# Kernel tuning notes

Measured on AMD Instinct MI355X. Metric: run time of the kernel, lower is better.

The kernel has to match this reference:

```python
import jax, jax.numpy as jnp
import numpy as np
import math

HID = 300   # model dim (d_k in the source's scale factor)
HDIM = 64   # attention projection dim
NH = 8      # heads = last axis of view(B,S,HDIM//8,8)
DH = HDIM // NH
L = 6


def pos_encoding(S, d):
    pos = jnp.arange(S, dtype=jnp.float32)[:, None]
    i = jnp.arange(d)
    expo = jnp.where(i % 2 == 0, i, i - 1).astype(jnp.float32) / d
    ang = pos / jnp.power(jnp.float32(10000.0), expo)  # (S, d)
    return jnp.where(i % 2 == 0, jnp.sin(ang), jnp.cos(ang))


def norm(x, g, b):
    mu = jnp.mean(x, axis=-1, keepdims=True)
    var = jnp.var(x, axis=-1, keepdims=True, ddof=1)  # torch.var is unbiased
    return g * (x - mu) / jnp.sqrt(var + 1e-8) + b


def mha(x, mask, wq, wk, wv, wo):
    B, S, _ = x.shape
    # view(B,S,DH,NH).permute(3,0,1,2): head h = feature indices i*NH+h
    q = (x @ wq).reshape(B, S, DH, NH).transpose(3, 0, 1, 2)  # (NH,B,S,DH)
    k = (x @ wk).reshape(B, S, DH, NH).transpose(3, 0, 1, 2)
    v = (x @ wv).reshape(B, S, DH, NH).transpose(3, 0, 1, 2)
    e = jnp.einsum('hbqd,hbkd->hbqk', q, k) / math.sqrt(HID)
    e = jnp.where(mask[None], jnp.float32(-1e9), e)
    alpha = jax.nn.softmax(e, axis=-1)
    h = jnp.einsum('hbqk,hbkd->hbqd', alpha, v)
    # cat(head0..head7, dim=2) -> head-major feature layout
    a = h.transpose(1, 2, 0, 3).reshape(B, S, HDIM)
    return a @ wo


def encoder(x, mask, wq, wk, wv, wo, w1, bb1, w2, bb2, g1, be1, g2, be2):
    x2 = mha(x, mask, wq, wk, wv, wo)
    x = norm(x2 + x, g1, be1)
    ff = jnp.maximum(x @ w1 + bb1, 0.0) @ w2 + bb2
    x = norm(ff + x, g2, be2)
    return x


def setup_inputs() -> dict:
    key = jax.random.key(0)
    ks = jax.random.split(key, 16)
    B, S, V, C = 32, 512, 50000, 1000
    sc = 0.02
    return {
        'x': jax.random.randint(ks[0], (B, S), 0, V),
        'emb': jax.random.normal(ks[1], (V, HID), jnp.float32) * sc,
        'WQ': jax.random.normal(ks[2], (L, HID, HDIM), jnp.float32) * sc,
        'WK': jax.random.normal(ks[3], (L, HID, HDIM), jnp.float32) * sc,
        'WV': jax.random.normal(ks[4], (L, HID, HDIM), jnp.float32) * sc,
        'WO': jax.random.normal(ks[5], (L, HDIM, HID), jnp.float32) * sc,
        'W1': jax.random.normal(ks[6], (L, HID, 4 * HID), jnp.float32) * sc,
        'b1': jax.random.normal(ks[7], (L, 4 * HID), jnp.float32) * sc,
        'W2': jax.random.normal(ks[8], (L, 4 * HID, HID), jnp.float32) * sc,
        'b2': jax.random.normal(ks[9], (L, HID), jnp.float32) * sc,
        'gamma1': jnp.ones((L,), jnp.float32),
        'beta1': jnp.zeros((L,), jnp.float32),
        'gamma2': jnp.ones((L,), jnp.float32),
        'beta2': jnp.zeros((L,), jnp.float32),
        'V_d': jax.random.normal(ks[10], (HID, C), jnp.float32) * sc,
        'gamma_f': jnp.float32(1.0),
        'beta_f': jnp.float32(0.0),
    }


def reference(x, emb, WQ, WK, WV, WO, W1, b1, W2, b2,
              gamma1, beta1, gamma2, beta2, V_d, gamma_f, beta_f):
    B, S = x.shape
    mask = (x == 0)[:, None, :] * jnp.ones((1, S, 1), bool)  # (B,S,S)
    x1 = emb[x]                               # (B,S,HID)
    x2 = x1 + pos_encoding(S, HID)[None]
    acc = x2 + x1                             # dense residual running sum
    out = x2
    for l in range(L):
        out = encoder(acc, mask, WQ[l], WK[l], WV[l], WO[l],
                      W1[l], b1[l], W2[l], b2[l],
                      gamma1[l], beta1[l], gamma2[l], beta2[l])
        acc = acc + out
    logits = jnp.sum(out, axis=1) @ V_d       # (B,C)
    return jax.nn.softmax(norm(logits, gamma_f, beta_f), axis=1)
```

## Files before the change

kernel.cpp:

```cpp
#include <hip/hip_runtime.h>
#include <hip/hip_bf16.h>
#include <cstdio>
#include <cstdint>

#define BATCH 32
#define SEQ 512
#define BSQ (BATCH*SEQ)
#define HIDD 300
#define HD 64
#define NHEAD 8
#define DHEAD 8
#define NLAYERS 6
#define FFD 1200
#define NCLS 1000
#define NSPLIT 4
#define KCH (SEQ/NSPLIT)
#define CLS_KS 4
#define CLS_KC (HIDD/CLS_KS)

typedef short short8 __attribute__((ext_vector_type(8)));
typedef float floatx4 __attribute__((ext_vector_type(4)));

__device__ __forceinline__ short f2b(float v){
  __hip_bfloat16 h = __float2bfloat16(v);
  short s; __builtin_memcpy(&s, &h, 2); return s;
}
__device__ __forceinline__ unsigned pk2(float a, float b){
  return (unsigned)(unsigned short)f2b(a) | ((unsigned)(unsigned short)f2b(b) << 16);
}

__global__ void t10_embed(const int* __restrict__ toks,
                          const float* __restrict__ emb,
                          float* __restrict__ acc,
                          short* __restrict__ accbf){
  int idx = blockIdx.x*256 + threadIdx.x;
  if (idx >= BSQ*320) return;
  int row = idx / 320;
  int j   = idx - row*320;
  if (j >= HIDD){ accbf[(size_t)row*320 + j] = 0; return; }
  int t = toks[row];
  float e = emb[(size_t)t*HIDD + j];
  int s = row & (SEQ-1);
  float expo = (float)(j & ~1) * (1.0f/(float)HIDD);
  float ang  = (float)s * expf(-expo * 9.210340371976184f);
  float pe   = (j & 1) ? cosf(ang) : sinf(ang);
  float v = 2.0f*e + pe;
  acc[(size_t)row*HIDD + j] = v;
  accbf[(size_t)row*320 + j] = f2b(v);
}

__global__ void prep_w(const float* __restrict__ src, short* __restrict__ dst,
                       int K, int N, int Kpad, int rows, int nbase,
                       int sls, int dls, int total, int perm){
  int idx = blockIdx.x*256 + threadIdx.x;
  if (idx >= total) return;
  int l   = idx / (rows*Kpad);
  int rem = idx - l*(rows*Kpad);
  int n = rem / Kpad;
  int k = rem - n*Kpad;
  int sc = perm ? ((n & 7)*8 + (n >> 3)) : n;
  float v = (n < N && k < K) ? src[(size_t)l*sls + (size_t)k*N + sc] : 0.f;
  dst[(size_t)l*dls + (size_t)(nbase+n)*Kpad + k] = f2b(v);
}

__global__ __launch_bounds__(256) void mm_a16(
    const short* __restrict__ A, const short* __restrict__ Wt,
    const float* __restrict__ bias, float* __restrict__ C,
    short* __restrict__ Cb,
    int M, int N, int Kpad, int Npad, int nnb, int relu){
  __shared__ short sA[64][40];
  __shared__ short sB[64][40];
  int wg = blockIdx.x;
  int cpx = gridDim.x >> 3;
  int swz = (wg & 7)*cpx + (wg >> 3);
  int mt = swz / nnb, nt = swz - mt*nnb;
  int m0 = mt*64, n0 = nt*64;
  int tid = threadIdx.x;
  int lane = tid & 63, wv = tid >> 6;
  int wm = (wv & 1)*32, wn = (wv >> 1)*32;
  int l15 = lane & 15, quad = lane >> 4;
  floatx4 acc[2][2] = {};
  int srow = tid >> 2, sko = (tid & 3)*8;
  const short* Arow = A  + (size_t)(m0 + srow)*Kpad + sko;
  const short* Brow = Wt + (size_t)(n0 + srow)*Kpad + sko;
  int nch = Kpad >> 5;
  for (int c = 0; c < nch; c++){
    int k0 = c*32;
    __syncthreads();
    *(short8*)&sA[srow][sko] = *(const short8*)(Arow + k0);
    *(short8*)&sB[srow][sko] = *(const short8*)(Brow + k0);
    __syncthreads();
    short8 af[2], bf[2];
    for (int i=0;i<2;i++)
      af[i] = *(const short8*)&sA[wm + i*16 + l15][quad*8];
    for (int j=0;j<2;j++)
      bf[j] = *(const short8*)&sB[wn + j*16 + l15][quad*8];
    for (int i=0;i<2;i++)
      for (int j=0;j<2;j++)
        acc[i][j] = __builtin_amdgcn_mfma_f32_16x16x32_bf16(af[i], bf[j], acc[i][j], 0,0,0);
  }
  if (Cb){
    for (int j=0;j<2;j++){
      int n = n0 + wn + j*16 + l15;
      float bv = (bias && n < N) ? bias[n] : 0.f;
      for (int i=0;i<2;i++){
        int mbase = m0 + wm + i*16 + quad*4;
        for (int r=0;r<4;r++){
          float cv = acc[i][j][r] + bv;
          if (relu) cv = fmaxf(cv, 0.f);
          Cb[(size_t)(mbase+r)*Npad + n] = (n < N) ? f2b(cv) : (short)0;
        }
      }
    }
  } else {
    for (int j=0;j<2;j++){
      int n = n0 + wn + j*16 + l15;
      if (n >= N) continue;
      float bv = bias ? bias[n] : 0.f;
      for (int i=0;i<2;i++){
        int mbase = m0 + wm + i*16 + quad*4;
        for (int r=0;r<4;r++){
          float cv = acc[i][j][r] + bv;
          if (relu) cv = fmaxf(cv, 0.f);
          C[(size_t)(mbase+r)*N + n] = cv;
        }
      }
    }
  }
}

__global__ __launch_bounds__(256) void mm64(
    const short* __restrict__ A, const short* __restrict__ Wt,
    const float* __restrict__ bias, float* __restrict__ C,
    short* __restrict__ Cb,
    int M, int N, int Kpad, int Npad, int nnb, int relu){
  __shared__ short sA[64][40];
  __shared__ short sB[128][40];
  int wg = blockIdx.x;
  int cpx = gridDim.x >> 3;
  int swz = (wg & 7)*cpx + (wg >> 3);
  int mt = swz / nnb, nt = swz - mt*nnb;
  int m0 = mt*64, n0 = nt*128;
  int tid = threadIdx.x;
  int lane = tid & 63, wv = tid >> 6;
  int l15 = lane & 15, quad = lane >> 4;
  int wn = wv*32;
  floatx4 acc[4][2] = {};
  int lr = tid >> 2, lc = (tid & 3)*8;
  const short* Arow  = A  + (size_t)(m0 + lr)*Kpad + lc;
  const short* Brow0 = Wt + (size_t)(n0 + lr)*Kpad + lc;
  const short* Brow1 = Wt + (size_t)(n0 + 64 + lr)*Kpad + lc;
  int nch = Kpad >> 5;
  for (int c = 0; c < nch; c++){
    int k0 = c*32;
    short8 va  = *(const short8*)(Arow  + k0);
    short8 vb0 = *(const short8*)(Brow0 + k0);
    short8 vb1 = *(const short8*)(Brow1 + k0);
    __syncthreads();
    *(short8*)&sA[lr][lc]      = va;
    *(short8*)&sB[lr][lc]      = vb0;
    *(short8*)&sB[64+lr][lc]   = vb1;
    __syncthreads();
    short8 af[4], bf[2];
    #pragma unroll
    for (int i=0;i<4;i++)
      af[i] = *(const short8*)&sA[i*16 + l15][quad*8];
    #pragma unroll
    for (int j=0;j<2;j++)
      bf[j] = *(const short8*)&sB[wn + j*16 + l15][quad*8];
    #pragma unroll
    for (int i=0;i<4;i++)
      #pragma unroll
      for (int j=0;j<2;j++)
        acc[i][j] = __builtin_amdgcn_mfma_f32_16x16x32_bf16(af[i], bf[j], acc[i][j], 0,0,0);
  }
  if (Cb){
    #pragma unroll
    for (int j=0;j<2;j++){
      int n = n0 + wn + j*16 + l15;
      float bv = (bias && n < N) ? bias[n] : 0.f;
      #pragma unroll
      for (int i=0;i<4;i++){
        int mbase = m0 + i*16 + quad*4;
        #pragma unroll
        for (int r=0;r<4;r++){
          float cv = acc[i][j][r] + bv;
          if (relu) cv = fmaxf(cv, 0.f);
          Cb[(size_t)(mbase+r)*Npad + n] = (n < N) ? f2b(cv) : (short)0;
        }
      }
    }
  } else {
    #pragma unroll
    for (int j=0;j<2;j++){
      int n = n0 + wn + j*16 + l15;
      if (n >= N) continue;
      float bv = bias ? bias[n] : 0.f;
      #pragma unroll
      for (int i=0;i<4;i++){
        int mbase = m0 + i*16 + quad*4;
        #pragma unroll
        for (int r=0;r<4;r++){
          float cv = acc[i][j][r] + bv;
          if (relu) cv = fmaxf(cv, 0.f);
          C[(size_t)(mbase+r)*N + n] = cv;
        }
      }
    }
  }
}

__global__ __launch_bounds__(256) void mm128p(
    const short* __restrict__ A, const short* __restrict__ Wt,
    const float* __restrict__ bias, float* __restrict__ C,
    short* __restrict__ Cb,
    int M, int N, int Kpad, int Npad, int nnb, int relu){
  __shared__ short sA[128][40];
  __shared__ short sB[128][40];
  int wg = blockIdx.x;
  int cpx = gridDim.x >> 3;
  int swz = (wg & 7)*cpx + (wg >> 3);
  int mt = swz / nnb, nt = swz - mt*nnb;
  int m0 = mt*128, n0 = nt*128;
  int tid = threadIdx.x;
  int lane = tid & 63, wv = tid >> 6;
  int wm = (wv & 1)*64, wn = (wv >> 1)*64;
  int l15 = lane & 15, quad = lane >> 4;
  floatx4 acc[4][4] = {};
  int lr = tid >> 2, lc = (tid & 3)*8;
  const short* Arow0 = A  + (size_t)(m0 + lr)*Kpad + lc;
  const short* Arow1 = A  + (size_t)(m0 + 64 + lr)*Kpad + lc;
  const short* Brow0 = Wt + (size_t)(n0 + lr)*Kpad + lc;
  const short* Brow1 = Wt + (size_t)(n0 + 64 + lr)*Kpad + lc;
  int nch = Kpad >> 5;
  for (int c = 0; c < nch; c++){
    int k0 = c*32;
    short8 va0 = *(const short8*)(Arow0 + k0);
    short8 va1 = *(const short8*)(Arow1 + k0);
    short8 vb0 = *(const short8*)(Brow0 + k0);
    short8 vb1 = *(const short8*)(Brow1 + k0);
    __syncthreads();
    *(short8*)&sA[lr][lc]    = va0;
    *(short8*)&sA[64+lr][lc] = va1;
    *(short8*)&sB[lr][lc]    = vb0;
    *(short8*)&sB[64+lr][lc] = vb1;
    __syncthreads();
    short8 af[4], bf[4];
    #pragma unroll
    for (int i=0;i<4;i++)
      af[i] = *(const short8*)&sA[wm + i*16 + l15][quad*8];
    #pragma unroll
    for (int j=0;j<4;j++)
      bf[j] = *(const short8*)&sB[wn + j*16 + l15][quad*8];
    #pragma unroll
    for (int i=0;i<4;i++)
      #pragma unroll
      for (int j=0;j<4;j++)
        acc[i][j] = __builtin_amdgcn_mfma_f32_16x16x32_bf16(af[i], bf[j], acc[i][j], 0,0,0);
  }
  if (Cb){
    #pragma unroll
    for (int j=0;j<4;j++){
      int n = n0 + wn + j*16 + l15;
      float bv = (bias && n < N) ? bias[n] : 0.f;
      #pragma unroll
      for (int i=0;i<4;i++){
        int mbase = m0 + wm + i*16 + quad*4;
        #pragma unroll
        for (int r=0;r<4;r++){
          float cv = acc[i][j][r] + bv;
          if (relu) cv = fmaxf(cv, 0.f);
          Cb[(size_t)(mbase+r)*Npad + n] = (n < N) ? f2b(cv) : (short)0;
        }
      }
    }
  } else {
    #pragma unroll
    for (int j=0;j<4;j++){
      int n = n0 + wn + j*16 + l15;
      if (n >= N) continue;
      float bv = bias ? bias[n] : 0.f;
      #pragma unroll
      for (int i=0;i<4;i++){
        int mbase = m0 + wm + i*16 + quad*4;
        #pragma unroll
        for (int r=0;r<4;r++){
          float cv = acc[i][j][r] + bv;
          if (relu) cv = fmaxf(cv, 0.f);
          C[(size_t)(mbase+r)*N + n] = cv;
        }
      }
    }
  }
}

__global__ __launch_bounds__(256) void t14_attn(
    const float* __restrict__ qkv, const int* __restrict__ toks,
    float* __restrict__ pp, float* __restrict__ ps){
  __shared__ float kb[KCH][9];
  __shared__ float vb[KCH][9];
  __shared__ float msk[KCH];
  __shared__ short Pl[4][16][136];
  int blk = blockIdx.x;
  int ks = blk & (NSPLIT-1);
  int bh = blk >> 2;
  int b = bh >> 3, h = bh & 7;
  int tid = threadIdx.x;
  int lane = tid & 63, w = tid >> 6;
  int quad = lane >> 4, l15 = lane & 15;
  int kbase = ks*KCH;
  {
    int r = tid >> 1, half = (tid & 1)*4;
    const float* src = qkv + (size_t)(b*SEQ + kbase + r)*192 + h*8 + half;
    float4 kx = *(const float4*)(src + 64);
    float4 vx = *(const float4*)(src + 128);
    kb[r][half+0]=kx.x; kb[r][half+1]=kx.y; kb[r][half+2]=kx.z; kb[r][half+3]=kx.w;
    vb[r][half+0]=vx.x; vb[r][half+1]=vx.y; vb[r][half+2]=vx.z; vb[r][half+3]=vx.w;
  }
  if (tid < KCH)
    msk[tid] = (toks[b*SEQ + kbase + tid]==0) ? -1e9f : 0.f;
  __syncthreads();

  short8 kfrag[8];
  #pragma unroll
  for (int kt=0;kt<8;kt++){
    short8 f;
    #pragma unroll
    for (int j=0;j<8;j++) f[j] = 0;
    if (quad == 0){
      #pragma unroll
      for (int j=0;j<8;j++) f[j] = f2b(kb[kt*16 + l15][j]);
    }
    kfrag[kt] = f;
  }
  short8 vfrag[4];
  #pragma unroll
  for (int ks2=0;ks2<4;ks2++){
    short8 f;
    #pragma unroll
    for (int j=0;j<8;j++) f[j] = 0;
    if (l15 < 8){
      #pragma unroll
      for (int j=0;j<8;j++) f[j] = f2b(vb[ks2*32 + quad*8 + j][l15]);
    } else if (l15 == 8){
      #pragma unroll
      for (int j=0;j<8;j++) f[j] = (short)0x3F80;
    }
    vfrag[ks2] = f;
  }
  const float scale = 0.057735026918962574f;

  for (int t = 0; t < 8; t++){
    int q0 = w*128 + t*16;
    short8 qf;
    #pragma unroll
    for (int j=0;j<8;j++) qf[j] = 0;
    if (quad == 0){
      const float* qsrc = qkv + (size_t)(b*SEQ + q0 + l15)*192 + h*8;
      float4 a = *(const float4*)qsrc;
      float4 c = *(const float4*)(qsrc + 4);
      qf[0]=f2b(a.x*scale); qf[1]=f2b(a.y*scale); qf[2]=f2b(a.z*scale); qf[3]=f2b(a.w*scale);
      qf[4]=f2b(c.x*scale); qf[5]=f2b(c.y*scale); qf[6]=f2b(c.z*scale); qf[7]=f2b(c.w*scale);
    }
    #pragma unroll
    for (int kt2 = 0; kt2 < 4; kt2++){
      floatx4 z = {0.f,0.f,0.f,0.f};
      floatx4 a0 = __builtin_amdgcn_mfma_f32_16x16x32_bf16(kfrag[2*kt2],   qf, z, 0,0,0);
      floatx4 a1 = __builtin_amdgcn_mfma_f32_16x16x32_bf16(kfrag[2*kt2+1], qf, z, 0,0,0);
      float p0[4], p1[4];
      #pragma unroll
      for (int r=0;r<4;r++){
        float m0 = msk[(2*kt2)*16   + quad*4 + r];
        float m1 = msk[(2*kt2+1)*16 + quad*4 + r];
        p0[r] = __expf(fminf(a0[r] + m0, 60.f));
        p1[r] = __expf(fminf(a1[r] + m1, 60.f));
      }
      uint2 u0, u1;
      u0.x = pk2(p0[0], p0[1]); u0.y = pk2(p0[2], p0[3]);
      u1.x = pk2(p1[0], p1[1]); u1.y = pk2(p1[2], p1[3]);
      *(uint2*)&Pl[w][l15][(2*kt2)*16   + quad*4] = u0;
      *(uint2*)&Pl[w][l15][(2*kt2+1)*16 + quad*4] = u1;
    }
    floatx4 o = {0.f,0.f,0.f,0.f};
    #pragma unroll
    for (int ks2=0; ks2<4; ks2++){
      short8 pa = *(const short8*)&Pl[w][l15][ks2*32 + quad*8];
      o = __builtin_amdgcn_mfma_f32_16x16x32_bf16(pa, vfrag[ks2], o, 0,0,0);
    }
    if (l15 < 8){
      #pragma unroll
      for (int r=0;r<4;r++){
        int q = q0 + quad*4 + r;
        pp[(size_t)ks*BSQ*64 + (size_t)(b*SEQ+q)*64 + h*8 + l15] = o[r];
      }
    } else if (l15 == 8){
      #pragma unroll
      for (int r=0;r<4;r++){
        int q = q0 + quad*4 + r;
        ps[(size_t)ks*BSQ*8 + (size_t)(b*SEQ+q)*8 + h] = o[r];
      }
    }
  }
}

__global__ __launch_bounds__(256) void t12_attn_comb(
    const float* __restrict__ pp, const float* __restrict__ ps,
    short* __restrict__ aout){
  int idx = blockIdx.x*256 + threadIdx.x;
  if (idx >= BSQ*8) return;
  float s = 0.f;
  for (int k=0;k<NSPLIT;k++) s += ps[(size_t)k*BSQ*8 + idx];
  float inv = 1.f/s;
  int bsq = idx >> 3, h = idx & 7;
  size_t base = (size_t)bsq*64 + h*8;
  float o[8] = {};
  for (int k=0;k<NSPLIT;k++){
    const float4* p = (const float4*)(pp + (size_t)k*BSQ*64 + base);
    float4 a = p[0], bq = p[1];
    o[0]+=a.x; o[1]+=a.y; o[2]+=a.z; o[3]+=a.w;
    o[4]+=bq.x; o[5]+=bq.y; o[6]+=bq.z; o[7]+=bq.w;
  }
  short8 r;
  for (int d=0;d<8;d++) r[d] = f2b(o[d]*inv);
  *(short8*)(aout + base) = r;
}

__global__ __launch_bounds__(256) void t10_addnorm(
                 const float* __restrict__ xa, const float* __restrict__ xb,
                 float* __restrict__ y, short* __restrict__ ybf,
                 float* __restrict__ accum, short* __restrict__ accbf,
                 const float* __restrict__ gamma, const float* __restrict__ beta,
                 int l){
  __shared__ float red[8];
  int row = blockIdx.x, tid = threadIdx.x;
  size_t base = (size_t)row*HIDD;
  size_t bbase = (size_t)row*320;
  float v0 = xa[base+tid] + xb[base+tid];
  float v1 = 0.f;
  int has1 = (tid+256 < HIDD);
  if (has1) v1 = xa[base+tid+256] + xb[base+tid+256];
  float s = v0+v1, sq = v0*v0+v1*v1;
  for (int off=32; off; off>>=1){ s += __shfl_down(s,off); sq += __shfl_down(sq,off); }
  int lane = tid & 63, w = tid >> 6;
  if (lane==0){ red[w]=s; red[4+w]=sq; }
  __syncthreads();
  float sum = red[0]+red[1]+red[2]+red[3];
  float ssq = red[4]+red[5]+red[6]+red[7];
  float mu  = sum * (1.0f/HIDD);
  float var = (ssq - (float)HIDD*mu*mu) * (1.0f/(HIDD-1));
  float rstd = rsqrtf(var + 1e-8f);
  float g = gamma[l], be = beta[l];
  float o0 = g*(v0-mu)*rstd + be;
  if (y) y[base+tid] = o0;
  if (ybf) ybf[bbase+tid] = f2b(o0);
  if (accum){
    float a0 = accum[base+tid] + o0;
    accum[base+tid] = a0;
    if (accbf) accbf[bbase+tid] = f2b(a0);
  }
  if (has1){
    float o1 = g*(v1-mu)*rstd + be;
    if (y) y[base+tid+256] = o1;
    if (ybf) ybf[bbase+tid+256] = f2b(o1);
    if (accum){
      float a1 = accum[base+tid+256] + o1;
      accum[base+tid+256] = a1;
      if (accbf) accbf[bbase+tid+256] = f2b(a1);
    }
  } else if (tid+256 < 320){
    if (ybf) ybf[bbase+tid+256] = 0;
    if (accbf) accbf[bbase+tid+256] = 0;
  }
}

__global__ __launch_bounds__(256) void t13_colsum_part(
    const float* __restrict__ outb, float* __restrict__ part){
  int blk = blockIdx.x;
  int b = blk >> 3, c = blk & 7;
  int tid = threadIdx.x;
  size_t base = (size_t)b*SEQ*HIDD + (size_t)c*64*HIDD;
  int j1 = tid + 256;
  float s0 = 0.f, s1 = 0.f;
  for (int t = 0; t < 64; t++){
    const float* row = outb + base + (size_t)t*HIDD;
    s0 += row[tid];
    if (j1 < HIDD) s1 += row[j1];
  }
  float* dst = part + (size_t)(c*BATCH + b)*HIDD;
  dst[tid] = s0;
  if (j1 < HIDD) dst[j1] = s1;
}

__global__ void t13_colsum_comb(const float* __restrict__ part,
                                float* __restrict__ sums){
  int idx = blockIdx.x*256 + threadIdx.x;
  if (idx >= BATCH*HIDD) return;
  float s = 0.f;
  for (int c = 0; c < 8; c++) s += part[(size_t)c*BATCH*HIDD + idx];
  sums[idx] = s;
}

__global__ __launch_bounds__(256) void t13_cls(
    const float* __restrict__ sums, const float* __restrict__ W,
    float* __restrict__ plog){
  int gid = blockIdx.x*256 + threadIdx.x;
  if (gid >= CLS_KS*BATCH*NCLS) return;
  int c = gid / (BATCH*NCLS);
  int rem = gid - c*(BATCH*NCLS);
  int m = rem / NCLS, n = rem - m*NCLS;
  const float* arow = sums + m*HIDD + c*CLS_KC;
  const float* wcol = W + (size_t)c*CLS_KC*NCLS + n;
  float acc = 0.f;
  #pragma unroll 5
  for (int k = 0; k < CLS_KC; k++)
    acc = fmaf(arow[k], wcol[(size_t)k*NCLS], acc);
  plog[gid] = acc;
}

__device__ __forceinline__ float t10_bsum(float val, float* red){
  for (int off=32; off; off>>=1) val += __shfl_down(val, off);
  __syncthreads();
  if ((threadIdx.x & 63)==0) red[threadIdx.x>>6] = val;
  __syncthreads();
  return red[0]+red[1]+red[2]+red[3];
}
__device__ __forceinline__ float t10_bmax(float val, float* red){
  for (int off=32; off; off>>=1) val = fmaxf(val, __shfl_down(val, off));
  __syncthreads();
  if ((threadIdx.x & 63)==0) red[threadIdx.x>>6] = val;
  __syncthreads();
  return fmaxf(fmaxf(red[0],red[1]), fmaxf(red[2],red[3]));
}

__global__ __launch_bounds__(256) void t10_final(
                  const float* __restrict__ plog,
                  const float* __restrict__ gf, const float* __restrict__ bff,
                  float* __restrict__ outp){
  __shared__ float red[4];
  int b = blockIdx.x, tid = threadIdx.x;
  size_t base = (size_t)b*NCLS;
  float v[4];
  float s = 0.f, sq = 0.f;
  for (int t=0;t<4;t++){
    int j = tid + t*256;
    float x = 0.f;
    if (j < NCLS){
      for (int c=0;c<CLS_KS;c++) x += plog[(size_t)c*BATCH*NCLS + base + j];
    }
    v[t] = x; s += x; sq += x*x;
  }
  s  = t10_bsum(s, red);
  sq = t10_bsum(sq, red);
  float mu  = s * (1.0f/NCLS);
  float var = (sq - (float)NCLS*mu*mu) * (1.0f/(NCLS-1));
  float rstd = rsqrtf(var + 1e-8f);
  float g = gf[0], be = bff[0];
  float y[4]; float mx = -1e30f;
  for (int t=0;t<4;t++){
    int j = tid + t*256;
    y[t] = g*(v[t]-mu)*rstd + be;
    if (j < NCLS) mx = fmaxf(mx, y[t]);
  }
  mx = t10_bmax(mx, red);
  float p[4]; float es = 0.f;
  for (int t=0;t<4;t++){
    int j = tid + t*256;
    p[t] = (j < NCLS) ? __expf(y[t]-mx) : 0.f;
    es += p[t];
  }
  es = t10_bsum(es, red);
  float inv = 1.0f/es;
  for (int t=0;t<4;t++){
    int j = tid + t*256;
    if (j < NCLS) outp[base+j] = p[t]*inv;
  }
}

extern "C" void kernel_launch(void* const* d_in, const int* in_sizes, int n_in,
                              void* d_out, int out_size, void* d_ws, size_t ws_size,
                              hipStream_t stream){
  const int*   toks = (const int*)d_in[0];
  const float* emb  = (const float*)d_in[1];
  const float* WQ   = (const float*)d_in[2];
  const float* WK   = (const float*)d_in[3];
  const float* WV   = (const float*)d_in[4];
  const float* WO   = (const float*)d_in[5];
  const float* W1   = (const float*)d_in[6];
  const float* b1   = (const float*)d_in[7];
  const float* W2   = (const float*)d_in[8];
  const float* b2   = (const float*)d_in[9];
  const float* g1   = (const float*)d_in[10];
  const float* be1  = (const float*)d_in[11];
  const float* g2   = (const float*)d_in[12];
  const float* be2  = (const float*)d_in[13];
  const float* Vd   = (const float*)d_in[14];
  const float* gf   = (const float*)d_in[15];
  const float* bff  = (const float*)d_in[16];
  float* outp = (float*)d_out;

  float* acc    = (float*)d_ws;
  float* xn     = acc    + (size_t)BSQ*HIDD;
  float* outb   = xn     + (size_t)BSQ*HIDD;
  float* tmp    = outb   + (size_t)BSQ*HIDD;
  float* qkv    = tmp    + (size_t)BSQ*HIDD;
  float* sums   = qkv    + (size_t)BSQ*192;
  float* logits = sums   + BATCH*HIDD;
  float* pp     = tmp;
  float* ps     = tmp + (size_t)NSPLIT*BSQ*64;
  short* acc_bf = (short*)(logits + BATCH*NCLS);
  short* xn_bf  = acc_bf + (size_t)BSQ*320;
  short* aat_bf = xn_bf  + (size_t)BSQ*320;
  short* ff1_bf = aat_bf + (size_t)BSQ*64;
  short* wqkv = ff1_bf + (size_t)BSQ*1280;
  short* wo   = wqkv + (size_t)6*256*320;
  short* w1t  = wo   + (size_t)6*384*64;
  short* w2t  = w1t  + (size_t)6*1280*320;
  float* cspart = (float*)(w2t + (size_t)6*384*1280);
  float* plog   = cspart + (size_t)8*BATCH*HIDD;

  {
    int tq = 6*64*320;
    prep_w<<<(tq+255)/256,256,0,stream>>>(WQ, wqkv, 300, 64, 320, 64, 0,   19200, 81920, tq, 1);
    prep_w<<<(tq+255)/256,256,0,stream>>>(WK, wqkv, 300, 64, 320, 64, 64,  19200, 81920, tq, 1);
    prep_w<<<(tq+255)/256,256,0,stream>>>(WV, wqkv, 300, 64, 320, 64, 128, 19200, 81920, tq, 1);
    prep_w<<<(tq+255)/256,256,0,stream>>>(WQ, wqkv, 300, 0,  320, 64, 192, 19200, 81920, tq, 0);
    int to = 6*384*64;
    prep_w<<<(to+255)/256,256,0,stream>>>(WO, wo, 64, 300, 64, 384, 0, 19200, 24576, to, 0);
    int t1 = 6*1280*320;
    prep_w<<<(t1+255)/256,256,0,stream>>>(W1, w1t, 300, 1200, 320, 1280, 0, 360000, 409600, t1, 0);
    int t2 = 6*384*1280;
    prep_w<<<(t2+255)/256,256,0,stream>>>(W2, w2t, 1200, 300, 1280, 384, 0, 360000, 491520, t2, 0);
  }

  t10_embed<<<(BSQ*320+255)/256, 256, 0, stream>>>(toks, emb, acc, acc_bf);

  for (int l = 0; l < NLAYERS; l++){
    mm64<<<256*2,256,0,stream>>>(acc_bf, wqkv + (size_t)l*81920, nullptr, qkv, nullptr,
                                 BSQ, 192, 320, 0, 2, 0);
    t14_attn<<<BATCH*NHEAD*NSPLIT, 256, 0, stream>>>(qkv, toks, pp, ps);
    t12_attn_comb<<<(BSQ*8)/256, 256, 0, stream>>>(pp, ps, aat_bf);
    mm_a16<<<256*5,256,0,stream>>>(aat_bf, wo + (size_t)l*24576, nullptr, tmp, nullptr,
                                   BSQ, 300, 64, 0, 5, 0);
    t10_addnorm<<<BSQ,256,0,stream>>>(tmp, acc, xn, xn_bf, nullptr, nullptr, g1, be1, l);
    mm128p<<<128*10,256,0,stream>>>(xn_bf, w1t + (size_t)l*409600, b1 + (size_t)l*FFD,
                                    nullptr, ff1_bf, BSQ, 1200, 320, 1280, 10, 1);
    mm64<<<256*3,256,0,stream>>>(ff1_bf, w2t + (size_t)l*491520, b2 + (size_t)l*HIDD,
                                 tmp, nullptr, BSQ, 300, 1280, 0, 3, 0);
    t10_addnorm<<<BSQ,256,0,stream>>>(tmp, xn, (l==NLAYERS-1)?outb:nullptr, nullptr,
                                      (l==NLAYERS-1)?nullptr:acc,
                                      (l==NLAYERS-1)?nullptr:acc_bf, g2, be2, l);
  }

  t13_colsum_part<<<BATCH*8, 256, 0, stream>>>(outb, cspart);
  t13_colsum_comb<<<(BATCH*HIDD+255)/256, 256, 0, stream>>>(cspart, sums);
  t13_cls<<<(CLS_KS*BATCH*NCLS)/256, 256, 0, stream>>>(sums, Vd, plog);
  t10_final<<<BATCH, 256, 0, stream>>>(plog, gf, bff, outp);

  hipStreamCaptureStatus cs = hipStreamCaptureStatusNone;
  hipStreamIsCapturing(stream, &cs);
  if (cs == hipStreamCaptureStatusNone){
    hipError_t e_sync = hipStreamSynchronize(stream);
    float ho[4] = {-1,-1,-1,-1};
    hipMemcpy(ho, d_out, 16, hipMemcpyDeviceToHost);
    fprintf(stderr, "[t17] sync=%s out[0..3]=%g,%g,%g,%g\n",
            hipGetErrorString(e_sync), ho[0], ho[1], ho[2], ho[3]);
    fflush(stderr);
  }
}
```

Measured before the change: 1.121 ms.

## Emit QKV as bf16, fold softmax scale into WK, warp-per-row addnorm

The QKV projection GEMM now writes bf16 output with a 256-column padded stride instead of fp32. Attention loads Q/K fragments directly as bf16 vectors and stages only V in shared memory. The 1/sqrt(d) scale is folded into the WK weights during prep, which removes the per-element scale and conversion in the attention inner loop. The add+layernorm kernel now handles one row per wavefront with shuffle-only reductions, four rows per block, dropping the shared-memory barrier. Rounding K·scale to bf16 slightly changes numerics.

```diff
diff --git a/kernel.cpp b/kernel.cpp
--- a/kernel.cpp
+++ b/kernel.cpp
@@ -15,6 +15,7 @@
 #define NCLS 1000
 #define NSPLIT 4
 #define KCH (SEQ/NSPLIT)
+#define QKVP 256
 #define CLS_KS 4
 #define CLS_KC (HIDD/CLS_KS)
 
@@ -51,7 +52,7 @@
 
 __global__ void prep_w(const float* __restrict__ src, short* __restrict__ dst,
                        int K, int N, int Kpad, int rows, int nbase,
-                       int sls, int dls, int total, int perm){
+                       int sls, int dls, int total, int perm, float smul){
   int idx = blockIdx.x*256 + threadIdx.x;
   if (idx >= total) return;
   int l   = idx / (rows*Kpad);
@@ -59,7 +60,7 @@
   int n = rem / Kpad;
   int k = rem - n*Kpad;
   int sc = perm ? ((n & 7)*8 + (n >> 3)) : n;
-  float v = (n < N && k < K) ? src[(size_t)l*sls + (size_t)k*N + sc] : 0.f;
+  float v = (n < N && k < K) ? src[(size_t)l*sls + (size_t)k*N + sc]*smul : 0.f;
   dst[(size_t)l*dls + (size_t)(nbase+n)*Kpad + k] = f2b(v);
 }
 
@@ -294,11 +295,10 @@
   }
 }
 
-__global__ __launch_bounds__(256) void t14_attn(
-    const float* __restrict__ qkv, const int* __restrict__ toks,
+__global__ __launch_bounds__(256) void t18_attn(
+    const short* __restrict__ qkvb, const int* __restrict__ toks,
     float* __restrict__ pp, float* __restrict__ ps){
-  __shared__ float kb[KCH][9];
-  __shared__ float vb[KCH][9];
+  __shared__ short vb16[KCH][16];
   __shared__ float msk[KCH];
   __shared__ short Pl[4][16][136];
   int blk = blockIdx.x;
@@ -309,16 +309,13 @@
   int lane = tid & 63, w = tid >> 6;
   int quad = lane >> 4, l15 = lane & 15;
   int kbase = ks*KCH;
-  {
-    int r = tid >> 1, half = (tid & 1)*4;
-    const float* src = qkv + (size_t)(b*SEQ + kbase + r)*192 + h*8 + half;
-    float4 kx = *(const float4*)(src + 64);
-    float4 vx = *(const float4*)(src + 128);
-    kb[r][half+0]=kx.x; kb[r][half+1]=kx.y; kb[r][half+2]=kx.z; kb[r][half+3]=kx.w;
-    vb[r][half+0]=vx.x; vb[r][half+1]=vx.y; vb[r][half+2]=vx.z; vb[r][half+3]=vx.w;
-  }
-  if (tid < KCH)
-    msk[tid] = (toks[b*SEQ + kbase + tid]==0) ? -1e9f : 0.f;
+  if (tid < KCH){
+    *(short8*)&vb16[tid][0] =
+      *(const short8*)(qkvb + (size_t)(b*SEQ + kbase + tid)*QKVP + 128 + h*8);
+  } else {
+    int r = tid - KCH;
+    msk[r] = (toks[b*SEQ + kbase + r]==0) ? -1e9f : 0.f;
+  }
   __syncthreads();
 
   short8 kfrag[8];
@@ -327,10 +324,8 @@
     short8 f;
     #pragma unroll
     for (int j=0;j<8;j++) f[j] = 0;
-    if (quad == 0){
-      #pragma unroll
-      for (int j=0;j<8;j++) f[j] = f2b(kb[kt*16 + l15][j]);
-    }
+    if (quad == 0)
+      f = *(const short8*)(qkvb + (size_t)(b*SEQ + kbase + kt*16 + l15)*QKVP + 64 + h*8);
     kfrag[kt] = f;
   }
   short8 vfrag[4];
@@ -341,27 +336,21 @@
     for (int j=0;j<8;j++) f[j] = 0;
     if (l15 < 8){
       #pragma unroll
-      for (int j=0;j<8;j++) f[j] = f2b(vb[ks2*32 + quad*8 + j][l15]);
+      for (int j=0;j<8;j++) f[j] = vb16[ks2*32 + quad*8 + j][l15];
     } else if (l15 == 8){
       #pragma unroll
       for (int j=0;j<8;j++) f[j] = (short)0x3F80;
     }
     vfrag[ks2] = f;
   }
-  const float scale = 0.057735026918962574f;
 
   for (int t = 0; t < 8; t++){
     int q0 = w*128 + t*16;
     short8 qf;
     #pragma unroll
     for (int j=0;j<8;j++) qf[j] = 0;
-    if (quad == 0){
-      const float* qsrc = qkv + (size_t)(b*SEQ + q0 + l15)*192 + h*8;
-      float4 a = *(const float4*)qsrc;
-      float4 c = *(const float4*)(qsrc + 4);
-      qf[0]=f2b(a.x*scale); qf[1]=f2b(a.y*scale); qf[2]=f2b(a.z*scale); qf[3]=f2b(a.w*scale);
-      qf[4]=f2b(c.x*scale); qf[5]=f2b(c.y*scale); qf[6]=f2b(c.z*scale); qf[7]=f2b(c.w*scale);
-    }
+    if (quad == 0)
+      qf = *(const short8*)(qkvb + (size_t)(b*SEQ + q0 + l15)*QKVP + h*8);
     #pragma unroll
     for (int kt2 = 0; kt2 < 4; kt2++){
       floatx4 z = {0.f,0.f,0.f,0.f};
@@ -425,51 +414,47 @@
   *(short8*)(aout + base) = r;
 }
 
-__global__ __launch_bounds__(256) void t10_addnorm(
+__global__ __launch_bounds__(256) void t18_addnorm(
                  const float* __restrict__ xa, const float* __restrict__ xb,
                  float* __restrict__ y, short* __restrict__ ybf,
                  float* __restrict__ accum, short* __restrict__ accbf,
                  const float* __restrict__ gamma, const float* __restrict__ beta,
                  int l){
-  __shared__ float red[8];
-  int row = blockIdx.x, tid = threadIdx.x;
-  size_t base = (size_t)row*HIDD;
+  int w = threadIdx.x >> 6, lane = threadIdx.x & 63;
+  int row = blockIdx.x*4 + w;
+  size_t base  = (size_t)row*HIDD;
   size_t bbase = (size_t)row*320;
-  float v0 = xa[base+tid] + xb[base+tid];
-  float v1 = 0.f;
-  int has1 = (tid+256 < HIDD);
-  if (has1) v1 = xa[base+tid+256] + xb[base+tid+256];
-  float s = v0+v1, sq = v0*v0+v1*v1;
+  float v[5];
+  float s = 0.f, sq = 0.f;
+  #pragma unroll
+  for (int t=0;t<5;t++){
+    int j = lane + t*64;
+    float x = (j < HIDD) ? xa[base+j] + xb[base+j] : 0.f;
+    v[t] = x; s += x; sq += x*x;
+  }
+  #pragma unroll
   for (int off=32; off; off>>=1){ s += __shfl_down(s,off); sq += __shfl_down(sq,off); }
-  int lane = tid & 63, w = tid >> 6;
-  if (lane==0){ red[w]=s; red[4+w]=sq; }
-  __syncthreads();
-  float sum = red[0]+red[1]+red[2]+red[3];
-  float ssq = red[4]+red[5]+red[6]+red[7];
-  float mu  = sum * (1.0f/HIDD);
-  float var = (ssq - (float)HIDD*mu*mu) * (1.0f/(HIDD-1));
+  s = __shfl(s, 0); sq = __shfl(sq, 0);
+  float mu  = s * (1.0f/HIDD);
+  float var = (sq - (float)HIDD*mu*mu) * (1.0f/(HIDD-1));
   float rstd = rsqrtf(var + 1e-8f);
   float g = gamma[l], be = beta[l];
-  float o0 = g*(v0-mu)*rstd + be;
-  if (y) y[base+tid] = o0;
-  if (ybf) ybf[bbase+tid] = f2b(o0);
-  if (accum){
-    float a0 = accum[base+tid] + o0;
-    accum[base+tid] = a0;
-    if (accbf) accbf[bbase+tid] = f2b(a0);
-  }
-  if (has1){
-    float o1 = g*(v1-mu)*rstd + be;
-    if (y) y[base+tid+256] = o1;
-    if (ybf) ybf[bbase+tid+256] = f2b(o1);
-    if (accum){
-      float a1 = accum[base+tid+256] + o1;
-      accum[base+tid+256] = a1;
-      if (accbf) accbf[bbase+tid+256] = f2b(a1);
-    }
-  } else if (tid+256 < 320){
-    if (ybf) ybf[bbase+tid+256] = 0;
-    if (accbf) accbf[bbase+tid+256] = 0;
+  #pragma unroll
+  for (int t=0;t<5;t++){
+    int j = lane + t*64;
+    if (j < HIDD){
+      float o = g*(v[t]-mu)*rstd + be;
+      if (y) y[base+j] = o;
+      if (ybf) ybf[bbase+j] = f2b(o);
+      if (accum){
+        float a = accum[base+j] + o;
+        accum[base+j] = a;
+        if (accbf) accbf[bbase+j] = f2b(a);
+      }
+    } else if (j < 320){
+      if (ybf) ybf[bbase+j] = 0;
+      if (accbf) accbf[bbase+j] = 0;
+    }
   }
 }
 
@@ -605,6 +590,7 @@
   float* qkv    = tmp    + (size_t)BSQ*HIDD;
   float* sums   = qkv    + (size_t)BSQ*192;
   float* logits = sums   + BATCH*HIDD;
+  short* qkv_bf = (short*)qkv;
   float* pp     = tmp;
   float* ps     = tmp + (size_t)NSPLIT*BSQ*64;
   short* acc_bf = (short*)(logits + BATCH*NCLS);
@@ -619,36 +605,37 @@
   float* plog   = cspart + (size_t)8*BATCH*HIDD;
 
   {
+    const float kscale = 0.057735026918962574f;
     int tq = 6*64*320;
-    prep_w<<<(tq+255)/256,256,0,stream>>>(WQ, wqkv, 300, 64, 320, 64, 0,   19200, 81920, tq, 1);
-    prep_w<<<(tq+255)/256,256,0,stream>>>(WK, wqkv, 300, 64, 320, 64, 64,  19200, 81920, tq, 1);
-    prep_w<<<(tq+255)/256,256,0,stream>>>(WV, wqkv, 300, 64, 320, 64, 128, 19200, 81920, tq, 1);
-    prep_w<<<(tq+255)/256,256,0,stream>>>(WQ, wqkv, 300, 0,  320, 64, 192, 19200, 81920, tq, 0);
+    prep_w<<<(tq+255)/256,256,0,stream>>>(WQ, wqkv, 300, 64, 320, 64, 0,   19200, 81920, tq, 1, 1.0f);
+    prep_w<<<(tq+255)/256,256,0,stream>>>(WK, wqkv, 300, 64, 320, 64, 64,  19200, 81920, tq, 1, kscale);
+    prep_w<<<(tq+255)/256,256,0,stream>>>(WV, wqkv, 300, 64, 320, 64, 128, 19200, 81920, tq, 1, 1.0f);
+    prep_w<<<(tq+255)/256,256,0,stream>>>(WQ, wqkv, 300, 0,  320, 64, 192, 19200, 81920, tq, 0, 1.0f);
     int to = 6*384*64;
-    prep_w<<<(to+255)/256,256,0,stream>>>(WO, wo, 64, 300, 64, 384, 0, 19200, 24576, to, 0);
+    prep_w<<<(to+255)/256,256,0,stream>>>(WO, wo, 64, 300, 64, 384, 0, 19200, 24576, to, 0, 1.0f);
     int t1 = 6*1280*320;
-    prep_w<<<(t1+255)/256,256,0,stream>>>(W1, w1t, 300, 1200, 320, 1280, 0, 360000, 409600, t1, 0);
+    prep_w<<<(t1+255)/256,256,0,stream>>>(W1, w1t, 300, 1200, 320, 1280, 0, 360000, 409600, t1, 0, 1.0f);
     int t2 = 6*384*1280;
-    prep_w<<<(t2+255)/256,256,0,stream>>>(W2, w2t, 1200, 300, 1280, 384, 0, 360000, 491520, t2, 0);
+    prep_w<<<(t2+255)/256,256,0,stream>>>(W2, w2t, 1200, 300, 1280, 384, 0, 360000, 491520, t2, 0, 1.0f);
   }
 
   t10_embed<<<(BSQ*320+255)/256, 256, 0, stream>>>(toks, emb, acc, acc_bf);
 
   for (int l = 0; l < NLAYERS; l++){
-    mm64<<<256*2,256,0,stream>>>(acc_bf, wqkv + (size_t)l*81920, nullptr, qkv, nullptr,
-                                 BSQ, 192, 320, 0, 2, 0);
-    t14_attn<<<BATCH*NHEAD*NSPLIT, 256, 0, stream>>>(qkv, toks, pp, ps);
+    mm64<<<256*2,256,0,stream>>>(acc_bf, wqkv + (size_t)l*81920, nullptr, nullptr, qkv_bf,
+                                 BSQ, 192, 320, QKVP, 2, 0);
+    t18_attn<<<BATCH*NHEAD*NSPLIT, 256, 0, stream>>>(qkv_bf, toks, pp, ps);
     t12_attn_comb<<<(BSQ*8)/256, 256, 0, stream>>>(pp, ps, aat_bf);
     mm_a16<<<256*5,256,0,stream>>>(aat_bf, wo + (size_t)l*24576, nullptr, tmp, nullptr,
                                    BSQ, 300, 64, 0, 5, 0);
-    t10_addnorm<<<BSQ,256,0,stream>>>(tmp, acc, xn, xn_bf, nullptr, nullptr, g1, be1, l);
+    t18_addnorm<<<BSQ/4,256,0,stream>>>(tmp, acc, xn, xn_bf, nullptr, nullptr, g1, be1, l);
     mm128p<<<128*10,256,0,stream>>>(xn_bf, w1t + (size_t)l*409600, b1 + (size_t)l*FFD,
                                     nullptr, ff1_bf, BSQ, 1200, 320, 1280, 10, 1);
     mm64<<<256*3,256,0,stream>>>(ff1_bf, w2t + (size_t)l*491520, b2 + (size_t)l*HIDD,
                                  tmp, nullptr, BSQ, 300, 1280, 0, 3, 0);
-    t10_addnorm<<<BSQ,256,0,stream>>>(tmp, xn, (l==NLAYERS-1)?outb:nullptr, nullptr,
-                                      (l==NLAYERS-1)?nullptr:acc,
-                                      (l==NLAYERS-1)?nullptr:acc_bf, g2, be2, l);
+    t18_addnorm<<<BSQ/4,256,0,stream>>>(tmp, xn, (l==NLAYERS-1)?outb:nullptr, nullptr,
+                                        (l==NLAYERS-1)?nullptr:acc,
+                                        (l==NLAYERS-1)?nullptr:acc_bf, g2, be2, l);
   }
 
   t13_colsum_part<<<BATCH*8, 256, 0, stream>>>(outb, cspart);
@@ -662,7 +649,7 @@
     hipError_t e_sync = hipStreamSynchronize(stream);
     float ho[4] = {-1,-1,-1,-1};
     hipMemcpy(ho, d_out, 16, hipMemcpyDeviceToHost);
-    fprintf(stderr, "[t17] sync=%s out[0..3]=%g,%g,%g,%g\n",
+    fprintf(stderr, "[t18] sync=%s out[0..3]=%g,%g,%g,%g\n",
             hipGetErrorString(e_sync), ho[0], ho[1], ho[2], ho[3]);
     fflush(stderr);
   }
```

Measured after the change: 1.077 ms. 1.04x faster.
